# Performance work log

Hardware: AMD Instinct MI355X
Metric: run time of the kernel (lower is better)

## Reference

```python
import jax, jax.numpy as jnp
import numpy as np

EPS_NORM = 1e-12
EPS_ABS = 1e-12


def _stack3(x):
    # x: [B, T, C] -> [B, T, 3, C] with left-shift, identity, right-shift taps
    prev = jnp.pad(x[:, :-1, :], ((0, 0), (1, 0), (0, 0)))
    nxt = jnp.pad(x[:, 1:, :], ((0, 0), (0, 1), (0, 0)))
    return jnp.stack([prev, x, nxt], axis=2)


def _l2_norm(x, axis):
    # matches layer's l2_normal: sqrt(max(sum(x^2), eps)), keepdims
    sq = jnp.sum(jnp.square(x), axis=axis, keepdims=True)
    return jnp.sqrt(jnp.maximum(sq, EPS_NORM))


def setup_inputs() -> dict:
    key = jax.random.key(0)
    k1, k2 = jax.random.split(key)
    B, T, C, K, U = 32, 4096, 128, 3, 256
    inputs = jax.random.normal(k1, (B, T, C), dtype=jnp.float32)
    # glorot uniform for w: limit = sqrt(6/(fan_in+fan_out)) with fan_in=C*K, fan_out=U
    limit = np.sqrt(6.0 / (C * K + U)).astype(np.float32)
    w = jax.random.uniform(k2, (1, C * K, U), dtype=jnp.float32, minval=-limit, maxval=limit)
    b = jnp.zeros((U,), dtype=jnp.float32)
    p = jnp.ones((U,), dtype=jnp.float32)
    q = jnp.zeros((1,), dtype=jnp.float32)
    return {"inputs": inputs, "w": w, "b": b, "p": p, "q": q}


def reference(inputs, w, b, p, q):
    B, T, C = inputs.shape
    U = w.shape[-1]
    x = _stack3(inputs).reshape(B, T, 3 * C)          # [B, T, 3C] (tap-major, matches tf stack+reshape)
    q2 = jnp.square(q)                                 # [1]
    x_norm = _l2_norm(x, axis=2) + q2                  # [B, T, 1]
    w_norm = _l2_norm(w, axis=1) + q2                  # [1, 1, U]
    w2 = w[0]                                          # [3C, U]
    sign = jnp.sign(jnp.einsum('btk,ku->btu', x, w2))  # sign of raw matmul
    y = jnp.einsum('btk,ku->btu', x / x_norm, w2 / w_norm[0])
    y = jnp.abs(y) + EPS_ABS
    y = jnp.power(y, jnp.square(p))                    # broadcast over units
    y = sign * y + b
    return y
```

## Files before the change

### kernel.cpp

```cpp
#include <hip/hip_runtime.h>

typedef __attribute__((ext_vector_type(8))) short short8;
typedef __attribute__((ext_vector_type(4))) float f32x4;

#define T_DIM 4096
#define C_DIM 128
#define U_DIM 256
#define BM 128
#define NROWS 130
#define LDK 136

__device__ __forceinline__ unsigned short f2bf(float f) {
    unsigned int u = __float_as_uint(f);
    u += 0x7FFFu + ((u >> 16) & 1u);
    return (unsigned short)(u >> 16);
}

__global__ void prep_kernel(const float* __restrict__ w,
                            const float* __restrict__ b,
                            const float* __restrict__ p,
                            const float* __restrict__ q,
                            unsigned short* __restrict__ wfrag,
                            float* __restrict__ winv,
                            float* __restrict__ p2,
                            float* __restrict__ bc) {
    if (blockIdx.x < 48) {
        int idx = blockIdx.x * 256 + threadIdx.x;
        int l  = idx & 63;
        int nt = (idx >> 6) & 15;
        int ks = idx >> 10;
        int n  = nt * 16 + (l & 15);
        int k0 = ks * 32 + ((l >> 4) << 3);
        #pragma unroll
        for (int j = 0; j < 8; ++j) {
            wfrag[(size_t)idx * 8 + j] = f2bf(w[(k0 + j) * U_DIM + n]);
        }
    } else {
        int u = threadIdx.x;
        float ss = 0.f;
        for (int k = 0; k < 3 * C_DIM; ++k) {
            float v = w[k * U_DIM + u];
            ss += v * v;
        }
        float q2 = q[0] * q[0];
        winv[u] = 1.0f / (sqrtf(fmaxf(ss, 1e-12f)) + q2);
        float pv = p[u];
        p2[u] = pv * pv;
        bc[u] = b[u];
    }
}

__global__ __launch_bounds__(512, 4) void cossim_main(
        const float* __restrict__ inp,
        const unsigned short* __restrict__ wfrag,
        const float* __restrict__ winv,
        const float* __restrict__ p2g,
        const float* __restrict__ bg,
        const float* __restrict__ qg,
        float* __restrict__ out) {
    __shared__ unsigned short inp_s[NROWS][LDK];
    __shared__ float ss_s[NROWS];
    __shared__ float xninv_s[BM];

    const int tid  = threadIdx.x;
    const int bidx = blockIdx.x;
    const int bb   = bidx >> 5;
    const int t0   = (bidx & 31) * BM;

    {
        const int r0 = tid >> 5;
        const int lc = (tid & 31) * 4;
        float4 v[9];
        #pragma unroll
        for (int i = 0; i < 9; ++i) {
            int r = r0 + i * 16;
            int t = t0 + r - 1;
            float4 val = make_float4(0.f, 0.f, 0.f, 0.f);
            if (r < NROWS && t >= 0 && t < T_DIM) {
                val = *(const float4*)(inp + ((size_t)bb * T_DIM + t) * C_DIM + lc);
            }
            v[i] = val;
        }
        #pragma unroll
        for (int i = 0; i < 9; ++i) {
            int r = r0 + i * 16;
            if (r < NROWS) {
                float4 val = v[i];
                float part = val.x * val.x + val.y * val.y + val.z * val.z + val.w * val.w;
                #pragma unroll
                for (int o = 16; o > 0; o >>= 1) part += __shfl_xor(part, o, 32);
                if ((tid & 31) == 0) ss_s[r] = part;
                ushort4 sv;
                sv.x = f2bf(val.x); sv.y = f2bf(val.y);
                sv.z = f2bf(val.z); sv.w = f2bf(val.w);
                *(ushort4*)(&inp_s[r][lc]) = sv;
            }
        }
    }
    __syncthreads();
    if (tid < BM) {
        float s3 = ss_s[tid] + ss_s[tid + 1] + ss_s[tid + 2];
        float q2 = qg[0] * qg[0];
        xninv_s[tid] = 1.0f / (sqrtf(fmaxf(s3, 1e-12f)) + q2);
    }
    __syncthreads();

    const int wid = tid >> 6;
    const int l   = tid & 63;
    const int tw  = wid >> 2;
    const int uw  = wid & 3;
    const int l15 = l & 15;
    const int lg  = l >> 4;

    f32x4 acc[4][4];
    #pragma unroll
    for (int tf = 0; tf < 4; ++tf)
        #pragma unroll
        for (int uf = 0; uf < 4; ++uf)
            acc[tf][uf] = (f32x4){0.f, 0.f, 0.f, 0.f};

    const short8* wf = (const short8*)wfrag;

    #pragma unroll
    for (int ks = 0; ks < 12; ++ks) {
        const int tap = ks >> 2;
        const int c0  = (ks & 3) * 32 + lg * 8;
        short8 xv[4], wv[4];
        #pragma unroll
        for (int tf = 0; tf < 4; ++tf) {
            int row = tw * 64 + tf * 16 + l15 + tap;
            xv[tf] = *(const short8*)(&inp_s[row][c0]);
        }
        #pragma unroll
        for (int uf = 0; uf < 4; ++uf) {
            wv[uf] = wf[(size_t)(ks * 16 + uw * 4 + uf) * 64 + l];
        }
        #pragma unroll
        for (int tf = 0; tf < 4; ++tf)
            #pragma unroll
            for (int uf = 0; uf < 4; ++uf)
                acc[tf][uf] = __builtin_amdgcn_mfma_f32_16x16x32_bf16(
                    wv[uf], xv[tf], acc[tf][uf], 0, 0, 0);
    }

    #pragma unroll
    for (int tf = 0; tf < 4; ++tf) {
        int trow = tw * 64 + tf * 16 + l15;
        float xi = xninv_s[trow];
        float* orow = out + ((size_t)bb * T_DIM + t0 + trow) * U_DIM;
        #pragma unroll
        for (int uf = 0; uf < 4; ++uf) {
            int uc = uw * 64 + uf * 16 + lg * 4;
            f32x4 wiv = *(const f32x4*)(winv + uc);
            f32x4 ppv = *(const f32x4*)(p2g + uc);
            f32x4 bbv = *(const f32x4*)(bg + uc);
            f32x4 r;
            #pragma unroll
            for (int j = 0; j < 4; ++j) {
                float raw = acc[tf][uf][j];
                float y   = raw * xi * wiv[j];
                float ay  = fabsf(y) + 1e-12f;
                float pw  = ppv[j];
                float rr  = (pw == 1.0f) ? ay : exp2f(pw * __log2f(ay));
                r[j] = __builtin_copysignf(rr, raw) + bbv[j];
            }
            *(f32x4*)(orow + uc) = r;
        }
    }
}

extern "C" void kernel_launch(void* const* d_in, const int* in_sizes, int n_in,
                              void* d_out, int out_size, void* d_ws, size_t ws_size,
                              hipStream_t stream) {
    const float* inp = (const float*)d_in[0];
    const float* w   = (const float*)d_in[1];
    const float* b   = (const float*)d_in[2];
    const float* p   = (const float*)d_in[3];
    const float* q   = (const float*)d_in[4];
    float* out = (float*)d_out;

    unsigned short* wfrag = (unsigned short*)d_ws;
    float* winv = (float*)((char*)d_ws + 196608);
    float* p2   = winv + 256;
    float* bc   = p2 + 256;

    prep_kernel<<<49, 256, 0, stream>>>(w, b, p, q, wfrag, winv, p2, bc);
    cossim_main<<<1024, 512, 0, stream>>>(inp, wfrag, winv, p2, bc, q, out);
}
```

Baseline: 73.76 us.

## Halve row tile to 64 and double-buffer MFMA operand loads

Each block now covers 64 time rows with 256 threads (4 waves, each owning a 64-column slice of U), which doubles the grid to 2048 blocks and cuts the shared-memory halo footprint. The K loop is software-pipelined: the LDS input fragments and global weight fragments for the next k-step are loaded into a second register set while the MFMAs of the current step run. This is meant to hide load latency and raise occupancy. The cost is a larger halo fraction (2 extra rows per 64 instead of per 128), more weight-fragment reads per output row, and higher register pressure from the double buffers.

```diff
diff --git a/kernel.cpp b/kernel.cpp
--- a/kernel.cpp
+++ b/kernel.cpp
@@ -6,8 +6,8 @@
 #define T_DIM 4096
 #define C_DIM 128
 #define U_DIM 256
-#define BM 128
-#define NROWS 130
+#define BM 64
+#define NROWS 66
 #define LDK 136
 
 __device__ __forceinline__ unsigned short f2bf(float f) {
@@ -50,7 +50,29 @@
     }
 }
 
-__global__ __launch_bounds__(512, 4) void cossim_main(
+#define KLOAD(ks, xv, wv)                                                  \
+    do {                                                                   \
+        const int tap_ = (ks) >> 2;                                        \
+        const int c0_  = ((ks) & 3) * 32 + lg * 8;                         \
+        _Pragma("unroll")                                                  \
+        for (int tf = 0; tf < 4; ++tf)                                     \
+            xv[tf] = *(const short8*)(&inp_s[tf * 16 + l15 + tap_][c0_]);  \
+        _Pragma("unroll")                                                  \
+        for (int uf = 0; uf < 4; ++uf)                                     \
+            wv[uf] = wf[(size_t)((ks) * 16 + uw * 4 + uf) * 64 + l];       \
+    } while (0)
+
+#define KMFMA(xv, wv)                                                      \
+    do {                                                                   \
+        _Pragma("unroll")                                                  \
+        for (int tf = 0; tf < 4; ++tf)                                     \
+            _Pragma("unroll")                                              \
+            for (int uf = 0; uf < 4; ++uf)                                 \
+                acc[tf][uf] = __builtin_amdgcn_mfma_f32_16x16x32_bf16(     \
+                    wv[uf], xv[tf], acc[tf][uf], 0, 0, 0);                 \
+    } while (0)
+
+__global__ __launch_bounds__(256, 3) void cossim_main(
         const float* __restrict__ inp,
         const unsigned short* __restrict__ wfrag,
         const float* __restrict__ winv,
@@ -64,8 +86,8 @@
 
     const int tid  = threadIdx.x;
     const int bidx = blockIdx.x;
-    const int bb   = bidx >> 5;
-    const int t0   = (bidx & 31) * BM;
+    const int bb   = bidx >> 6;
+    const int t0   = (bidx & 63) * BM;
 
     {
         const int r0 = tid >> 5;
@@ -73,7 +95,7 @@
         float4 v[9];
         #pragma unroll
         for (int i = 0; i < 9; ++i) {
-            int r = r0 + i * 16;
+            int r = r0 + i * 8;
             int t = t0 + r - 1;
             float4 val = make_float4(0.f, 0.f, 0.f, 0.f);
             if (r < NROWS && t >= 0 && t < T_DIM) {
@@ -83,7 +105,7 @@
         }
         #pragma unroll
         for (int i = 0; i < 9; ++i) {
-            int r = r0 + i * 16;
+            int r = r0 + i * 8;
             if (r < NROWS) {
                 float4 val = v[i];
                 float part = val.x * val.x + val.y * val.y + val.z * val.z + val.w * val.w;
@@ -105,10 +127,8 @@
     }
     __syncthreads();
 
-    const int wid = tid >> 6;
+    const int uw  = tid >> 6;
     const int l   = tid & 63;
-    const int tw  = wid >> 2;
-    const int uw  = wid & 3;
     const int l15 = l & 15;
     const int lg  = l >> 4;
 
@@ -121,31 +141,22 @@
 
     const short8* wf = (const short8*)wfrag;
 
+    short8 xvA[4], wvA[4], xvB[4], wvB[4];
+    KLOAD(0, xvA, wvA);
     #pragma unroll
     for (int ks = 0; ks < 12; ++ks) {
-        const int tap = ks >> 2;
-        const int c0  = (ks & 3) * 32 + lg * 8;
-        short8 xv[4], wv[4];
-        #pragma unroll
-        for (int tf = 0; tf < 4; ++tf) {
-            int row = tw * 64 + tf * 16 + l15 + tap;
-            xv[tf] = *(const short8*)(&inp_s[row][c0]);
-        }
-        #pragma unroll
-        for (int uf = 0; uf < 4; ++uf) {
-            wv[uf] = wf[(size_t)(ks * 16 + uw * 4 + uf) * 64 + l];
-        }
-        #pragma unroll
-        for (int tf = 0; tf < 4; ++tf)
-            #pragma unroll
-            for (int uf = 0; uf < 4; ++uf)
-                acc[tf][uf] = __builtin_amdgcn_mfma_f32_16x16x32_bf16(
-                    wv[uf], xv[tf], acc[tf][uf], 0, 0, 0);
+        if ((ks & 1) == 0) {
+            if (ks < 11) KLOAD(ks + 1, xvB, wvB);
+            KMFMA(xvA, wvA);
+        } else {
+            if (ks < 11) KLOAD(ks + 1, xvA, wvA);
+            KMFMA(xvB, wvB);
+        }
     }
 
     #pragma unroll
     for (int tf = 0; tf < 4; ++tf) {
-        int trow = tw * 64 + tf * 16 + l15;
+        int trow = tf * 16 + l15;
         float xi = xninv_s[trow];
         float* orow = out + ((size_t)bb * T_DIM + t0 + trow) * U_DIM;
         #pragma unroll
@@ -185,5 +196,5 @@
     float* bc   = p2 + 256;
 
     prep_kernel<<<49, 256, 0, stream>>>(w, b, p, q, wfrag, winv, p2, bc);
-    cossim_main<<<1024, 512, 0, stream>>>(inp, wfrag, winv, p2, bc, q, out);
-}
+    cossim_main<<<2048, 256, 0, stream>>>(inp, wfrag, winv, p2, bc, q, out);
+}
```

After: 72.37 us. Within noise of the previous version (-1.9%).
